# Optimization experiments

Measured on AMD Instinct MI355X. Metric: run time of the kernel, lower is better.

## Reference

```python
import jax, jax.numpy as jnp
import numpy as np


def _maxpool2x2(x):
    # x: [B, C, H, W] -> [B, C, H//2, W//2], 2x2 max pool stride 2
    B, C, H, W = x.shape
    return x.reshape(B, C, H // 2, 2, W // 2, 2).max(axis=(3, 5))


def setup_inputs() -> dict:
    key = jax.random.key(0)
    ks = jax.random.split(key, 5)
    C = 64
    B, H, W = 16, 64, 64
    x = jax.random.normal(ks[0], (B, C, H, W), dtype=jnp.float32)
    s = 0.05
    W_theta = jax.random.normal(ks[1], (C // 8, C), dtype=jnp.float32) * s
    W_phi = jax.random.normal(ks[2], (C // 8, C), dtype=jnp.float32) * s
    W_g = jax.random.normal(ks[3], (C // 2, C), dtype=jnp.float32) * s
    W_attn = jax.random.normal(ks[4], (C, C // 2), dtype=jnp.float32) * s
    sigma = jnp.zeros((1,), dtype=jnp.float32)
    return {"x": x, "W_theta": W_theta, "W_phi": W_phi, "W_g": W_g,
            "W_attn": W_attn, "sigma": sigma}


def reference(x, W_theta, W_phi, W_g, W_attn, sigma):
    B, C, H, W = x.shape
    HW = H * W
    # 1x1 convs are channel GEMMs
    theta = jnp.einsum('oc,bchw->bohw', W_theta, x).reshape(B, C // 8, HW)
    phi = jnp.einsum('oc,bchw->bohw', W_phi, x)
    phi = _maxpool2x2(phi).reshape(B, C // 8, HW // 4)
    # attn: [B, HW, HW//4]
    attn = jax.nn.softmax(jnp.einsum('bcq,bck->bqk', theta, phi), axis=-1)
    g = jnp.einsum('oc,bchw->bohw', W_g, x)
    g = _maxpool2x2(g).reshape(B, C // 2, HW // 4)
    # attn_g: [B, C//2, HW]
    attn_g = jnp.einsum('bck,bqk->bcq', g, attn).reshape(B, C // 2, H, W)
    attn_g = jnp.einsum('oc,bchw->bohw', W_attn, attn_g)
    return x + sigma[0] * attn_g
```

## Files before the change

kernel.cpp:

```cpp
#include <hip/hip_runtime.h>
#include <math.h>

#define B_ 16
#define C_ 64
#define HW_ 4096
#define PHW_ 1024

typedef __attribute__((ext_vector_type(8))) short bf8;
typedef __attribute__((ext_vector_type(16))) float fv16;

union FU { bf8 v; unsigned u[4]; };

__device__ inline unsigned short f2bf(float f) {
    unsigned u = __float_as_uint(f);
    return (unsigned short)((u + 0x7FFFu + ((u >> 16) & 1u)) >> 16);
}
__device__ inline unsigned packbf(float a, float b) {
    return (unsigned)f2bf(a) | ((unsigned)f2bf(b) << 16);
}
__device__ inline unsigned packtr(float a, float b) {
    return (__float_as_uint(a) >> 16) | (__float_as_uint(b) & 0xFFFF0000u);
}

__global__ __launch_bounds__(256) void conv_stage(
    const float* __restrict__ x,
    const float* __restrict__ Wt,
    const float* __restrict__ Wp,
    const float* __restrict__ Wg,
    float* __restrict__ theta,
    unsigned short* __restrict__ phi_pack,
    unsigned short* __restrict__ g_pack)
{
    __shared__ float sx[64][128];
    __shared__ float sw[64][48];
    __shared__ float pool2[40][33];

    const int t  = threadIdx.x;
    const int b  = blockIdx.x >> 5;
    const int h2 = blockIdx.x & 31;

    for (int i = t; i < 3072; i += 256) {
        int c = i / 48, ch = i - c * 48;
        float v;
        if (ch < 8)       v = Wt[ch * 64 + c];
        else if (ch < 16) v = Wp[(ch - 8) * 64 + c];
        else              v = Wg[(ch - 16) * 64 + c];
        sw[c][ch] = v;
    }
    const float* xbase = x + (size_t)b * C_ * HW_ + h2 * 128;
    for (int f = t; f < 2048; f += 256) {
        int c = f >> 5, j4 = f & 31;
        *(float4*)&sx[c][j4 * 4] = *(const float4*)&xbase[(size_t)c * HW_ + j4 * 4];
    }
    __syncthreads();

    {
        const int px  = t & 127;
        const int ch0 = (t >> 7) * 4;
        float a0 = 0.f, a1 = 0.f, a2 = 0.f, a3 = 0.f;
        for (int c = 0; c < 64; c++) {
            float xv = sx[c][px];
            float4 wv = *(const float4*)&sw[c][ch0];
            a0 += wv.x * xv; a1 += wv.y * xv; a2 += wv.z * xv; a3 += wv.w * xv;
        }
        float* tp = theta + (size_t)b * 8 * HW_ + h2 * 128 + px;
        tp[(size_t)(ch0 + 0) * HW_] = a0;
        tp[(size_t)(ch0 + 1) * HW_] = a1;
        tp[(size_t)(ch0 + 2) * HW_] = a2;
        tp[(size_t)(ch0 + 3) * HW_] = a3;
    }

    {
        const int p   = t & 31;
        const int grp = t >> 5;
        float a[5][4];
#pragma unroll
        for (int j = 0; j < 5; j++)
#pragma unroll
            for (int u = 0; u < 4; u++) a[j][u] = 0.f;

        for (int c = 0; c < 64; c++) {
            float2 xa  = *(const float2*)&sx[c][2 * p];
            float2 xb2 = *(const float2*)&sx[c][64 + 2 * p];
#pragma unroll
            for (int j = 0; j < 5; j++) {
                float wv = sw[c][8 + grp * 5 + j];
                a[j][0] += wv * xa.x;  a[j][1] += wv * xa.y;
                a[j][2] += wv * xb2.x; a[j][3] += wv * xb2.y;
            }
        }
#pragma unroll
        for (int j = 0; j < 5; j++) {
            float m = fmaxf(fmaxf(a[j][0], a[j][1]), fmaxf(a[j][2], a[j][3]));
            pool2[grp * 5 + j][p] = m;
        }
    }
    __syncthreads();

    if (t < 64) {
        unsigned u0 = 0, u1 = 0, u2 = 0, u3 = 0;
        if (t < 32) {
            float v[8];
#pragma unroll
            for (int j = 0; j < 8; j++) v[j] = pool2[j][t];
            u0 = packbf(v[0], v[1]); u1 = packbf(v[2], v[3]);
            u2 = packbf(v[4], v[5]); u3 = packbf(v[6], v[7]);
        }
        uint4 pkt = make_uint4(u0, u1, u2, u3);
        *(uint4*)(phi_pack + ((size_t)((b * 32 + h2) * 64 + t)) * 8) = pkt;
    } else if (t < 192) {
        const int tt  = t - 64;
        const int ktl = tt >> 6;
        const int ln  = tt & 63;
        const int c   = ln & 31;
        const int hh  = ln >> 5;
        float v[8];
#pragma unroll
        for (int j = 0; j < 8; j++) v[j] = pool2[8 + c][ktl * 16 + hh * 8 + j];
        uint4 pkt = make_uint4(packbf(v[0], v[1]), packbf(v[2], v[3]),
                               packbf(v[4], v[5]), packbf(v[6], v[7]));
        *(uint4*)(g_pack + ((size_t)((b * 64 + h2 * 2 + ktl) * 64 + ln)) * 8) = pkt;
    }
}

__global__ __launch_bounds__(256, 4) void attn_mfma(
    const float* __restrict__ theta_g,
    const unsigned short* __restrict__ phi_pack,
    const unsigned short* __restrict__ g_pack,
    const float* __restrict__ Wa,
    const float* __restrict__ x,
    const float* __restrict__ sigma,
    float* __restrict__ out)
{
    __shared__ float comb[4][64][17];

    const int t = threadIdx.x, wave = t >> 6, lane = t & 63;
    const int lo = lane & 31, hi = lane >> 5;
    const int qtile = blockIdx.x * 2 + (wave >> 1);
    const int khalf = wave & 1;
    const int b = qtile >> 7, qt = qtile & 127;
    const int qg = qt * 32 + lo;

    FU tb; tb.u[0] = tb.u[1] = tb.u[2] = tb.u[3] = 0;
    if (hi == 0) {
        const float LOG2E = 1.4426950408889634f;
        float tv[8];
#pragma unroll
        for (int j = 0; j < 8; j++)
            tv[j] = theta_g[(((size_t)b * 8 + j) << 12) + qg] * LOG2E;
        tb.u[0] = packbf(tv[0], tv[1]); tb.u[1] = packbf(tv[2], tv[3]);
        tb.u[2] = packbf(tv[4], tv[5]); tb.u[3] = packbf(tv[6], tv[7]);
    }

    fv16 zf, acc;
#pragma unroll
    for (int r = 0; r < 16; r++) { zf[r] = 0.f; acc[r] = 0.f; }
    float ps = 0.f;

    const int kt0 = khalf * 16;
    for (int kt = kt0; kt < kt0 + 16; kt++) {
        FU pa;
        pa.v = *(const bf8*)(phi_pack + ((size_t)((b * 32 + kt) * 64 + lane)) * 8);
        fv16 s = __builtin_amdgcn_mfma_f32_32x32x16_bf16(pa.v, tb.v, zf, 0, 0, 0);

        float p[16];
#pragma unroll
        for (int r = 0; r < 16; r++) { p[r] = __builtin_amdgcn_exp2f(s[r]); ps += p[r]; }

        unsigned pk[8], qk[8];
#pragma unroll
        for (int i = 0; i < 8; i++) pk[i] = packtr(p[2 * i], p[2 * i + 1]);
#pragma unroll
        for (int i = 0; i < 8; i++) qk[i] = (unsigned)__shfl_xor((int)pk[i], 32);

        FU pb0, pb1;
        pb0.u[0] = hi ? qk[2] : pk[0]; pb0.u[1] = hi ? qk[3] : pk[1];
        pb0.u[2] = hi ? pk[2] : qk[0]; pb0.u[3] = hi ? pk[3] : qk[1];
        pb1.u[0] = hi ? qk[6] : pk[4]; pb1.u[1] = hi ? qk[7] : pk[5];
        pb1.u[2] = hi ? pk[6] : qk[4]; pb1.u[3] = hi ? pk[7] : qk[5];

        FU ga0, ga1;
        ga0.v = *(const bf8*)(g_pack + ((size_t)((b * 64 + kt * 2    ) * 64 + lane)) * 8);
        ga1.v = *(const bf8*)(g_pack + ((size_t)((b * 64 + kt * 2 + 1) * 64 + lane)) * 8);
        acc = __builtin_amdgcn_mfma_f32_32x32x16_bf16(ga0.v, pb0.v, acc, 0, 0, 0);
        acc = __builtin_amdgcn_mfma_f32_32x32x16_bf16(ga1.v, pb1.v, acc, 0, 0, 0);
    }

#pragma unroll
    for (int r = 0; r < 16; r++) comb[wave][lane][r] = acc[r];
    comb[wave][lane][16] = ps;
    __syncthreads();
    const int pw = wave ^ 1;
#pragma unroll
    for (int r = 0; r < 16; r++) acc[r] += comb[pw][lane][r];
    ps += comb[pw][lane][16];

    float lsum = ps + __shfl_xor(ps, 32);
    float inv = 1.f / lsum;

    float on[16];
#pragma unroll
    for (int r = 0; r < 16; r++) on[r] = acc[r] * inv;
    unsigned pk[8], qk[8];
#pragma unroll
    for (int i = 0; i < 8; i++) pk[i] = packtr(on[2 * i], on[2 * i + 1]);
#pragma unroll
    for (int i = 0; i < 8; i++) qk[i] = (unsigned)__shfl_xor((int)pk[i], 32);
    FU ob0, ob1;
    ob0.u[0] = hi ? qk[2] : pk[0]; ob0.u[1] = hi ? qk[3] : pk[1];
    ob0.u[2] = hi ? pk[2] : qk[0]; ob0.u[3] = hi ? pk[3] : qk[1];
    ob1.u[0] = hi ? qk[6] : pk[4]; ob1.u[1] = hi ? qk[7] : pk[5];
    ob1.u[2] = hi ? pk[6] : qk[4]; ob1.u[3] = hi ? pk[7] : qk[5];

    FU wa0, wa1;
    {
        const float* wr = Wa + (khalf * 32 + lo) * 32;
#pragma unroll
        for (int ktw = 0; ktw < 2; ktw++) {
            float w8[8];
#pragma unroll
            for (int j = 0; j < 8; j++) w8[j] = wr[ktw * 16 + hi * 8 + j];
            FU f;
            f.u[0] = packbf(w8[0], w8[1]); f.u[1] = packbf(w8[2], w8[3]);
            f.u[2] = packbf(w8[4], w8[5]); f.u[3] = packbf(w8[6], w8[7]);
            if (ktw == 0) wa0 = f; else wa1 = f;
        }
    }
    fv16 d2 = __builtin_amdgcn_mfma_f32_32x32x16_bf16(wa0.v, ob0.v, zf, 0, 0, 0);
    d2 = __builtin_amdgcn_mfma_f32_32x32x16_bf16(wa1.v, ob1.v, d2, 0, 0, 0);

    const float sig = sigma[0];
#pragma unroll
    for (int r = 0; r < 16; r++) {
        int row = (r & 3) + ((r >> 2) << 3) + (hi << 2);
        int o = khalf * 32 + row;
        size_t idx = (((size_t)b * 64 + o) << 12) + qg;
        out[idx] = x[idx] + sig * d2[r];
    }
}

extern "C" void kernel_launch(void* const* d_in, const int* in_sizes, int n_in,
                              void* d_out, int out_size, void* d_ws, size_t ws_size,
                              hipStream_t stream) {
    const float* x     = (const float*)d_in[0];
    const float* Wt    = (const float*)d_in[1];
    const float* Wp    = (const float*)d_in[2];
    const float* Wg    = (const float*)d_in[3];
    const float* Wa    = (const float*)d_in[4];
    const float* sigma = (const float*)d_in[5];
    float* out = (float*)d_out;

    float* theta = (float*)d_ws;
    unsigned short* phi_pack = (unsigned short*)(theta + (size_t)B_ * 8 * HW_);
    unsigned short* g_pack   = phi_pack + (size_t)B_ * 32 * 64 * 8;

    conv_stage<<<512, 256, 0, stream>>>(x, Wt, Wp, Wg, theta, phi_pack, g_pack);
    attn_mfma<<<1024, 256, 0, stream>>>(theta, phi_pack, g_pack, Wa, x, sigma, out);
}
```

Measured before the change: 111.1 us.

## Read conv weights via scalar loads and interleave exp with MFMA in attention loop

```diff
diff --git a/kernel.cpp b/kernel.cpp
--- a/kernel.cpp
+++ b/kernel.cpp
@@ -32,21 +32,12 @@
     unsigned short* __restrict__ g_pack)
 {
     __shared__ float sx[64][128];
-    __shared__ float sw[64][48];
     __shared__ float pool2[40][33];
 
     const int t  = threadIdx.x;
     const int b  = blockIdx.x >> 5;
     const int h2 = blockIdx.x & 31;
 
-    for (int i = t; i < 3072; i += 256) {
-        int c = i / 48, ch = i - c * 48;
-        float v;
-        if (ch < 8)       v = Wt[ch * 64 + c];
-        else if (ch < 16) v = Wp[(ch - 8) * 64 + c];
-        else              v = Wg[(ch - 16) * 64 + c];
-        sw[c][ch] = v;
-    }
     const float* xbase = x + (size_t)b * C_ * HW_ + h2 * 128;
     for (int f = t; f < 2048; f += 256) {
         int c = f >> 5, j4 = f & 31;
@@ -54,45 +45,47 @@
     }
     __syncthreads();
 
-    {
-        const int px  = t & 127;
-        const int ch0 = (t >> 7) * 4;
-        float a0 = 0.f, a1 = 0.f, a2 = 0.f, a3 = 0.f;
-        for (int c = 0; c < 64; c++) {
-            float xv = sx[c][px];
-            float4 wv = *(const float4*)&sw[c][ch0];
-            a0 += wv.x * xv; a1 += wv.y * xv; a2 += wv.z * xv; a3 += wv.w * xv;
-        }
-        float* tp = theta + (size_t)b * 8 * HW_ + h2 * 128 + px;
-        tp[(size_t)(ch0 + 0) * HW_] = a0;
-        tp[(size_t)(ch0 + 1) * HW_] = a1;
-        tp[(size_t)(ch0 + 2) * HW_] = a2;
-        tp[(size_t)(ch0 + 3) * HW_] = a3;
-    }
-
-    {
-        const int p   = t & 31;
-        const int grp = t >> 5;
-        float a[5][4];
-#pragma unroll
-        for (int j = 0; j < 5; j++)
-#pragma unroll
-            for (int u = 0; u < 4; u++) a[j][u] = 0.f;
-
-        for (int c = 0; c < 64; c++) {
-            float2 xa  = *(const float2*)&sx[c][2 * p];
-            float2 xb2 = *(const float2*)&sx[c][64 + 2 * p];
-#pragma unroll
-            for (int j = 0; j < 5; j++) {
-                float wv = sw[c][8 + grp * 5 + j];
-                a[j][0] += wv * xa.x;  a[j][1] += wv * xa.y;
-                a[j][2] += wv * xb2.x; a[j][3] += wv * xb2.y;
-            }
-        }
-#pragma unroll
-        for (int j = 0; j < 5; j++) {
-            float m = fmaxf(fmaxf(a[j][0], a[j][1]), fmaxf(a[j][2], a[j][3]));
-            pool2[grp * 5 + j][p] = m;
+    const int wv   = __builtin_amdgcn_readfirstlane(t >> 6);
+    const int lane = t & 63;
+    const int chbase = wv * 12;
+
+    const float* wrow[12];
+#pragma unroll
+    for (int j = 0; j < 12; j++) {
+        int gch = chbase + j;
+        wrow[j] = (gch < 8) ? (Wt + gch * 64)
+                : (gch < 16) ? (Wp + (gch - 8) * 64)
+                             : (Wg + (gch - 16) * 64);
+    }
+
+    float acc[12][2];
+#pragma unroll
+    for (int j = 0; j < 12; j++) { acc[j][0] = 0.f; acc[j][1] = 0.f; }
+
+    for (int c = 0; c < 64; c++) {
+        float2 xv = *(const float2*)&sx[c][2 * lane];
+#pragma unroll
+        for (int j = 0; j < 12; j++) {
+            float w = wrow[j][c];
+            acc[j][0] += w * xv.x;
+            acc[j][1] += w * xv.y;
+        }
+    }
+
+    if (wv == 0) {
+        float* tp = theta + (size_t)b * 8 * HW_ + h2 * 128 + 2 * lane;
+#pragma unroll
+        for (int j = 0; j < 8; j++)
+            *(float2*)&tp[(size_t)j * HW_] = make_float2(acc[j][0], acc[j][1]);
+    }
+
+#pragma unroll
+    for (int j = 0; j < 12; j++) {
+        int gch = chbase + j;
+        if (gch >= 8) {
+            float hm = fmaxf(acc[j][0], acc[j][1]);
+            float pm = fmaxf(hm, __shfl_xor(hm, 32));
+            if (lane < 32) pool2[gch - 8][lane] = pm;
         }
     }
     __syncthreads();
@@ -158,32 +151,49 @@
     float ps = 0.f;
 
     const int kt0 = khalf * 16;
-    for (int kt = kt0; kt < kt0 + 16; kt++) {
-        FU pa;
-        pa.v = *(const bf8*)(phi_pack + ((size_t)((b * 32 + kt) * 64 + lane)) * 8);
+    const unsigned short* phip = phi_pack + ((size_t)((b * 32 + kt0) * 64 + lane)) * 8;
+    const unsigned short* gp   = g_pack   + ((size_t)((b * 64 + kt0 * 2) * 64 + lane)) * 8;
+
+#pragma unroll 2
+    for (int i = 0; i < 16; i++) {
+        FU pa, ga0, ga1;
+        pa.v  = *(const bf8*)(phip + (size_t)i * 512);
+        ga0.v = *(const bf8*)(gp + (size_t)i * 1024);
+        ga1.v = *(const bf8*)(gp + (size_t)i * 1024 + 512);
         fv16 s = __builtin_amdgcn_mfma_f32_32x32x16_bf16(pa.v, tb.v, zf, 0, 0, 0);
 
-        float p[16];
-#pragma unroll
-        for (int r = 0; r < 16; r++) { p[r] = __builtin_amdgcn_exp2f(s[r]); ps += p[r]; }
-
-        unsigned pk[8], qk[8];
-#pragma unroll
-        for (int i = 0; i < 8; i++) pk[i] = packtr(p[2 * i], p[2 * i + 1]);
-#pragma unroll
-        for (int i = 0; i < 8; i++) qk[i] = (unsigned)__shfl_xor((int)pk[i], 32);
-
-        FU pb0, pb1;
-        pb0.u[0] = hi ? qk[2] : pk[0]; pb0.u[1] = hi ? qk[3] : pk[1];
-        pb0.u[2] = hi ? pk[2] : qk[0]; pb0.u[3] = hi ? pk[3] : qk[1];
-        pb1.u[0] = hi ? qk[6] : pk[4]; pb1.u[1] = hi ? qk[7] : pk[5];
-        pb1.u[2] = hi ? pk[6] : qk[4]; pb1.u[3] = hi ? pk[7] : qk[5];
-
-        FU ga0, ga1;
-        ga0.v = *(const bf8*)(g_pack + ((size_t)((b * 64 + kt * 2    ) * 64 + lane)) * 8);
-        ga1.v = *(const bf8*)(g_pack + ((size_t)((b * 64 + kt * 2 + 1) * 64 + lane)) * 8);
-        acc = __builtin_amdgcn_mfma_f32_32x32x16_bf16(ga0.v, pb0.v, acc, 0, 0, 0);
-        acc = __builtin_amdgcn_mfma_f32_32x32x16_bf16(ga1.v, pb1.v, acc, 0, 0, 0);
+        {
+            unsigned pk[4], qk[4];
+#pragma unroll
+            for (int u = 0; u < 4; u++) {
+                float p0 = __builtin_amdgcn_exp2f(s[2 * u]);
+                float p1 = __builtin_amdgcn_exp2f(s[2 * u + 1]);
+                ps += p0 + p1;
+                pk[u] = packtr(p0, p1);
+            }
+#pragma unroll
+            for (int u = 0; u < 4; u++) qk[u] = (unsigned)__shfl_xor((int)pk[u], 32);
+            FU pb;
+            pb.u[0] = hi ? qk[2] : pk[0]; pb.u[1] = hi ? qk[3] : pk[1];
+            pb.u[2] = hi ? pk[2] : qk[0]; pb.u[3] = hi ? pk[3] : qk[1];
+            acc = __builtin_amdgcn_mfma_f32_32x32x16_bf16(ga0.v, pb.v, acc, 0, 0, 0);
+        }
+        {
+            unsigned pk[4], qk[4];
+#pragma unroll
+            for (int u = 0; u < 4; u++) {
+                float p0 = __builtin_amdgcn_exp2f(s[8 + 2 * u]);
+                float p1 = __builtin_amdgcn_exp2f(s[9 + 2 * u]);
+                ps += p0 + p1;
+                pk[u] = packtr(p0, p1);
+            }
+#pragma unroll
+            for (int u = 0; u < 4; u++) qk[u] = (unsigned)__shfl_xor((int)pk[u], 32);
+            FU pb;
+            pb.u[0] = hi ? qk[2] : pk[0]; pb.u[1] = hi ? qk[3] : pk[1];
+            pb.u[2] = hi ? pk[2] : qk[0]; pb.u[3] = hi ? pk[3] : qk[1];
+            acc = __builtin_amdgcn_mfma_f32_32x32x16_bf16(ga1.v, pb.v, acc, 0, 0, 0);
+        }
     }
 
 #pragma unroll
```

Measured after the change: 108.0 us. 1.03x faster.
